# Optimization experiments

Measured on AMD Instinct MI355X. Metric: run time of the kernel, lower is better.

Reference implementation:

```python
import jax, jax.numpy as jnp
import numpy as np

N = 50000      # nodes
E = 1600000    # directed edges (before self-loops)
H = 4          # heads for conv2/conv3


def feast(x, src, dst, W, u, c, b, heads, out_ch):
    """PyG FeaStConv: q = softmax((x_j - x_i) @ u + c) over heads,
    msg = sum_h q_h * (x_j @ W_h), mean-aggregated over in-neighbors, + bias.
    src/dst already include self-loops."""
    xj = x[src]                                   # [E', in]
    xi = x[dst]                                   # [E', in]
    q = jax.nn.softmax((xj - xi) @ u + c, axis=1)            # [E', H]
    t = (xj @ W).reshape(-1, heads, out_ch)                  # [E', H, out]
    m = jnp.einsum('ehc,eh->ec', t, q)                       # [E', out]
    s = jax.ops.segment_sum(m, dst, num_segments=N)          # [N, out]
    deg = jax.ops.segment_sum(jnp.ones((src.shape[0],), x.dtype), dst, num_segments=N)
    return s / jnp.maximum(deg, 1.0)[:, None] + b


def _glorot(k, shape):
    fan_in, fan_out = shape[0], shape[1] if len(shape) > 1 else shape[0]
    lim = np.sqrt(6.0 / (fan_in + fan_out))
    return jax.random.uniform(k, shape, jnp.float32, -lim, lim)


def setup_inputs() -> dict:
    key = jax.random.key(0)
    ks = jax.random.split(key, 32)
    d = {}
    d['x'] = jax.random.normal(ks[0], (N, 16), jnp.float32)
    d['edge_index'] = jax.random.randint(ks[1], (2, E), 0, N, jnp.int32)
    # conv2: 16->16, H=4 ; conv3: 16->16, H=4
    d['W2'] = _glorot(ks[2], (16, H * 16)); d['u2'] = _glorot(ks[3], (16, H))
    d['c2'] = jnp.zeros((H,), jnp.float32); d['b2'] = jnp.zeros((16,), jnp.float32)
    d['W3'] = _glorot(ks[4], (16, H * 16)); d['u3'] = _glorot(ks[5], (16, H))
    d['c3'] = jnp.zeros((H,), jnp.float32); d['b3'] = jnp.zeros((16,), jnp.float32)
    # conv4: 16->16 H=1 ; conv5: 16->32 H=1 ; conv6: 32->64 H=1
    d['W4'] = _glorot(ks[6], (16, 16)); d['u4'] = _glorot(ks[7], (16, 1))
    d['c4'] = jnp.zeros((1,), jnp.float32); d['b4'] = jnp.zeros((16,), jnp.float32)
    d['W5'] = _glorot(ks[8], (16, 32)); d['u5'] = _glorot(ks[9], (16, 1))
    d['c5'] = jnp.zeros((1,), jnp.float32); d['b5'] = jnp.zeros((32,), jnp.float32)
    d['W6'] = _glorot(ks[10], (32, 64)); d['u6'] = _glorot(ks[11], (32, 1))
    d['c6'] = jnp.zeros((1,), jnp.float32); d['b6'] = jnp.zeros((64,), jnp.float32)
    # MLP head: 64->16->4->1
    d['lw1'] = _glorot(ks[12], (64, 16)); d['lb1'] = jnp.zeros((16,), jnp.float32)
    d['lw2'] = _glorot(ks[13], (16, 4));  d['lb2'] = jnp.zeros((4,), jnp.float32)
    d['lw3'] = _glorot(ks[14], (4, 1));   d['lb3'] = jnp.zeros((1,), jnp.float32)
    return d


def reference(x, edge_index, W2, u2, c2, b2, W3, u3, c3, b3, W4, u4, c4, b4,
               W5, u5, c5, b5, W6, u6, c6, b6, lw1, lb1, lw2, lb2, lw3, lb3):
    loop = jnp.arange(N, dtype=edge_index.dtype)
    src = jnp.concatenate([edge_index[0], loop])   # self-loops (PyG default)
    dst = jnp.concatenate([edge_index[1], loop])
    h = jax.nn.relu(x)
    h = jax.nn.relu(feast(h, src, dst, W2, u2, c2, b2, H, 16))
    h = jax.nn.relu(feast(h, src, dst, W3, u3, c3, b3, H, 16))
    h = jax.nn.relu(feast(h, src, dst, W4, u4, c4, b4, 1, 16))
    h = jax.nn.relu(feast(h, src, dst, W5, u5, c5, b5, 1, 32))
    h = jax.nn.relu(feast(h, src, dst, W6, u6, c6, b6, 1, 64))
    h = jax.nn.relu(h @ lw1 + lb1)   # dropout disabled (eval mode)
    h = jax.nn.relu(h @ lw2 + lb2)
    return jax.nn.sigmoid(h @ lw3 + lb3)
```

## Files before the change

kernel.cpp:

```cpp
#include <hip/hip_runtime.h>
#include <math.h>


#define CAP 96
#define NPB 256
#define BCAP 10240

__global__ void part_count(const int* __restrict__ dst, int E,
                           int* __restrict__ counts, int NB) {
    __shared__ int hist[256];
    for (int i = threadIdx.x; i < 256; i += blockDim.x) hist[i] = 0;
    __syncthreads();
    int nth = gridDim.x * blockDim.x;
    int tid = blockIdx.x * blockDim.x + threadIdx.x;
    int E4 = E >> 2;
    const int4* dst4 = (const int4*)dst;
    for (int e4 = tid; e4 < E4; e4 += nth) {
        int4 d = dst4[e4];
        atomicAdd(&hist[d.x >> 8], 1);
        atomicAdd(&hist[d.y >> 8], 1);
        atomicAdd(&hist[d.z >> 8], 1);
        atomicAdd(&hist[d.w >> 8], 1);
    }
    for (int e = (E4 << 2) + tid; e < E; e += nth)
        atomicAdd(&hist[dst[e] >> 8], 1);
    __syncthreads();
    for (int b = threadIdx.x; b < NB; b += blockDim.x)
        counts[b * NPB + blockIdx.x] = hist[b];
}

__global__ void part_scan(int* __restrict__ counts, int* __restrict__ bucketCnt) {
    __shared__ int s[NPB];
    int b = blockIdx.x;
    int t = threadIdx.x;
    int v = counts[b * NPB + t];
    s[t] = v;
    __syncthreads();
    for (int off = 1; off < NPB; off <<= 1) {
        int x = (t >= off) ? s[t - off] : 0;
        __syncthreads();
        s[t] += x;
        __syncthreads();
    }
    counts[b * NPB + t] = s[t] - v;
    if (t == NPB - 1) bucketCnt[b] = s[t];
}

__global__ void part_scatter(const int* __restrict__ src, const int* __restrict__ dst,
                             int E, const int* __restrict__ counts,
                             unsigned int* __restrict__ barr, int NB) {
    __shared__ int cur[256];
    for (int b = threadIdx.x; b < NB; b += blockDim.x)
        cur[b] = counts[b * NPB + blockIdx.x];
    __syncthreads();
    int nth = gridDim.x * blockDim.x;
    int tid = blockIdx.x * blockDim.x + threadIdx.x;
    int E4 = E >> 2;
    const int4* dst4 = (const int4*)dst;
    const int4* src4 = (const int4*)src;
    for (int e4 = tid; e4 < E4; e4 += nth) {
        int4 d = dst4[e4];
        int4 s = src4[e4];
        int p0 = atomicAdd(&cur[d.x >> 8], 1);
        barr[(size_t)(d.x >> 8) * BCAP + p0] = ((unsigned)(d.x & 255) << 16) | (unsigned)s.x;
        int p1 = atomicAdd(&cur[d.y >> 8], 1);
        barr[(size_t)(d.y >> 8) * BCAP + p1] = ((unsigned)(d.y & 255) << 16) | (unsigned)s.y;
        int p2 = atomicAdd(&cur[d.z >> 8], 1);
        barr[(size_t)(d.z >> 8) * BCAP + p2] = ((unsigned)(d.z & 255) << 16) | (unsigned)s.z;
        int p3 = atomicAdd(&cur[d.w >> 8], 1);
        barr[(size_t)(d.w >> 8) * BCAP + p3] = ((unsigned)(d.w & 255) << 16) | (unsigned)s.w;
    }
    for (int e = (E4 << 2) + tid; e < E; e += nth) {
        int d = dst[e];
        int pos = atomicAdd(&cur[d >> 8], 1);
        barr[(size_t)(d >> 8) * BCAP + pos] = ((unsigned)(d & 255) << 16) | (unsigned)src[e];
    }
}

__global__ void build_rows(const unsigned int* __restrict__ barr,
                           const int* __restrict__ bucketCnt,
                           int* __restrict__ padded, int* __restrict__ cnt, int N) {
    __shared__ int c[256];
    int b = blockIdx.x;
    int lo = b << 8;
    int nNodes = min(256, N - lo);
    for (int i = threadIdx.x; i < nNodes; i += blockDim.x) c[i] = 0;
    __syncthreads();
    int tot = bucketCnt[b];
    const unsigned int* be = barr + (size_t)b * BCAP;
    for (int e = threadIdx.x; e < tot; e += blockDim.x) {
        unsigned int pk = be[e];
        int dl = (int)(pk >> 16);
        int s  = (int)(pk & 0xFFFFu);
        int slot = atomicAdd(&c[dl], 1);
        padded[(size_t)(lo + dl) * CAP + slot] = s;
    }
    __syncthreads();
    for (int i = threadIdx.x; i < nNodes; i += blockDim.x) cnt[lo + i] = c[i];
}

template <bool RELU_IN>
__global__ void prep_h4(const float* __restrict__ h, const float* __restrict__ W,
                        const float* __restrict__ u, const float* __restrict__ cvec,
                        float4* __restrict__ Tt, float4* __restrict__ a4,
                        float4* __restrict__ b4, int N) {
    int t = blockIdx.x * blockDim.x + threadIdx.x;
    int i = t >> 4, c = t & 15;
    if (i >= N) return;
    const float4* hp = (const float4*)(h + (size_t)i * 16);
    float4 q0 = hp[0], q1 = hp[1], q2 = hp[2], q3 = hp[3];
    float hv[16] = {q0.x, q0.y, q0.z, q0.w, q1.x, q1.y, q1.z, q1.w,
                    q2.x, q2.y, q2.z, q2.w, q3.x, q3.y, q3.z, q3.w};
    if (RELU_IN) {
        #pragma unroll
        for (int k = 0; k < 16; ++k) hv[k] = fmaxf(hv[k], 0.f);
    }
    float4 tv = {0.f, 0.f, 0.f, 0.f};
    #pragma unroll
    for (int k = 0; k < 16; ++k) {
        const float* Wk = W + k * 64 + c;
        tv.x = fmaf(hv[k], Wk[0],  tv.x);
        tv.y = fmaf(hv[k], Wk[16], tv.y);
        tv.z = fmaf(hv[k], Wk[32], tv.z);
        tv.w = fmaf(hv[k], Wk[48], tv.w);
    }
    Tt[(size_t)i * 16 + c] = tv;
    float p0 = 0.f, p1 = 0.f, p2 = 0.f, p3 = 0.f;
    #pragma unroll
    for (int k = 0; k < 16; ++k) {
        const float* uk = u + k * 4;
        p0 = fmaf(hv[k], uk[0], p0);
        p1 = fmaf(hv[k], uk[1], p1);
        p2 = fmaf(hv[k], uk[2], p2);
        p3 = fmaf(hv[k], uk[3], p3);
    }
    if (c == 0) {
        float z0 = p0 + cvec[0], z1 = p1 + cvec[1];
        float z2 = p2 + cvec[2], z3 = p3 + cvec[3];
        float A = fmaxf(fmaxf(z0, z1), fmaxf(z2, z3));
        float4 av = {__expf(z0 - A), __expf(z1 - A), __expf(z2 - A), __expf(z3 - A)};
        a4[i] = av;
        float B = fminf(fminf(p0, p1), fminf(p2, p3));
        float4 bv = {__expf(B - p0), __expf(B - p1), __expf(B - p2), __expf(B - p3)};
        b4[i] = bv;
    }
}

__global__ void row_h4(const int* __restrict__ cnt, const int* __restrict__ padded,
                       const float4* __restrict__ a4, const float4* __restrict__ b4,
                       const float4* __restrict__ Tt, const float* __restrict__ bvec,
                       float* __restrict__ out, int N) {
    int wid = (blockIdx.x * blockDim.x + threadIdx.x) >> 6;
    int lane = threadIdx.x & 63;
    if (wid >= N) return;
    const int i = wid;
    const int j = lane >> 4, c = lane & 15;
    const int nE = cnt[i];
    const int base = i * CAP;
    const float4 bv = b4[i];
    float acc = 0.f;
    for (int e = j; e < nE; e += 4) {
        int s = padded[base + e];
        float4 av = a4[s];
        float4 tv = Tt[(size_t)s * 16 + c];
        float w0 = av.x * bv.x, w1 = av.y * bv.y;
        float w2 = av.z * bv.z, w3 = av.w * bv.w;
        float sum = (w0 + w1) + (w2 + w3);
        float inv = __builtin_amdgcn_rcpf(sum);
        float dot = fmaf(w0, tv.x, fmaf(w1, tv.y, fmaf(w2, tv.z, w3 * tv.w)));
        acc = fmaf(dot, inv, acc);
    }
    acc += __shfl_xor(acc, 16);
    acc += __shfl_xor(acc, 32);
    if (lane < 16) {
        float4 av = a4[i];
        float4 tv = Tt[(size_t)i * 16 + c];
        float w0 = av.x * bv.x, w1 = av.y * bv.y;
        float w2 = av.z * bv.z, w3 = av.w * bv.w;
        float sum = (w0 + w1) + (w2 + w3);
        float inv = __builtin_amdgcn_rcpf(sum);
        float sval = fmaf(w0, tv.x, fmaf(w1, tv.y, fmaf(w2, tv.z, w3 * tv.w))) * inv;
        out[(size_t)i * 16 + c] = fmaxf((acc + sval) / (float)(nE + 1) + bvec[c], 0.f);
    }
}

template <int IN, int OUT>
__global__ void row_lin(const int* __restrict__ cnt, const int* __restrict__ padded,
                        const float* __restrict__ h, const float* __restrict__ Wm,
                        const float* __restrict__ bvec, float* __restrict__ out, int N) {
    constexpr int QUADS = IN / 4;
    constexpr int GRPS = 64 / QUADS;
    int wid = (blockIdx.x * blockDim.x + threadIdx.x) >> 6;
    int lane = threadIdx.x & 63;
    if (wid >= N) return;
    const int i = wid;
    const int sub = lane & (QUADS - 1);
    const int g = lane / QUADS;
    const int nE = cnt[i];
    const int base = i * CAP;
    const float4* h4 = (const float4*)h;
    float4 acc = {0.f, 0.f, 0.f, 0.f};
    for (int e = g; e < nE; e += GRPS) {
        int s = padded[base + e];
        float4 v = h4[(size_t)s * QUADS + sub];
        acc.x += v.x; acc.y += v.y; acc.z += v.z; acc.w += v.w;
    }
    #pragma unroll
    for (int mask = QUADS; mask < 64; mask <<= 1) {
        acc.x += __shfl_xor(acc.x, mask);
        acc.y += __shfl_xor(acc.y, mask);
        acc.z += __shfl_xor(acc.z, mask);
        acc.w += __shfl_xor(acc.w, mask);
    }
    float invd = 1.0f / (float)(nE + 1);
    float4 sv = h4[(size_t)i * QUADS + sub];
    float4 m;
    m.x = (acc.x + sv.x) * invd;
    m.y = (acc.y + sv.y) * invd;
    m.z = (acc.z + sv.z) * invd;
    m.w = (acc.w + sv.w) * invd;
    int o = (lane < OUT) ? lane : 0;
    float oacc = bvec[o];
    #pragma unroll
    for (int q = 0; q < QUADS; ++q) {
        float m0 = __shfl(m.x, q);
        float m1 = __shfl(m.y, q);
        float m2 = __shfl(m.z, q);
        float m3 = __shfl(m.w, q);
        oacc = fmaf(m0, Wm[(4 * q + 0) * OUT + o], oacc);
        oacc = fmaf(m1, Wm[(4 * q + 1) * OUT + o], oacc);
        oacc = fmaf(m2, Wm[(4 * q + 2) * OUT + o], oacc);
        oacc = fmaf(m3, Wm[(4 * q + 3) * OUT + o], oacc);
    }
    if (lane < OUT) out[(size_t)i * OUT + lane] = fmaxf(oacc, 0.f);
}

__global__ void mlp_kernel(const float* __restrict__ h,
                           const float* __restrict__ lw1, const float* __restrict__ lb1,
                           const float* __restrict__ lw2, const float* __restrict__ lb2,
                           const float* __restrict__ lw3, const float* __restrict__ lb3,
                           float* __restrict__ out, int N) {
    int i = blockIdx.x * blockDim.x + threadIdx.x;
    if (i >= N) return;
    float a1[16];
    #pragma unroll
    for (int o = 0; o < 16; ++o) a1[o] = lb1[o];
    const float4* h4 = (const float4*)(h + (size_t)i * 64);
    #pragma unroll 4
    for (int k4 = 0; k4 < 16; ++k4) {
        float4 v = h4[k4];
        int k = k4 * 4;
        #pragma unroll
        for (int o = 0; o < 16; ++o) {
            a1[o] += v.x * lw1[(k + 0) * 16 + o];
            a1[o] += v.y * lw1[(k + 1) * 16 + o];
            a1[o] += v.z * lw1[(k + 2) * 16 + o];
            a1[o] += v.w * lw1[(k + 3) * 16 + o];
        }
    }
    float a2[4];
    #pragma unroll
    for (int j = 0; j < 4; ++j) a2[j] = lb2[j];
    #pragma unroll
    for (int o = 0; o < 16; ++o) {
        float v = fmaxf(a1[o], 0.f);
        #pragma unroll
        for (int j = 0; j < 4; ++j) a2[j] += v * lw2[o * 4 + j];
    }
    float z = lb3[0];
    #pragma unroll
    for (int j = 0; j < 4; ++j) z += fmaxf(a2[j], 0.f) * lw3[j];
    out[i] = 1.0f / (1.0f + __expf(-z));
}

extern "C" void kernel_launch(void* const* d_in, const int* in_sizes, int n_in,
                              void* d_out, int out_size, void* d_ws, size_t ws_size,
                              hipStream_t stream) {
    const float* x  = (const float*)d_in[0];
    const int*   ei = (const int*)d_in[1];
    const int E = in_sizes[1] / 2;
    const int N = in_sizes[0] / 16;
    const int* src = ei;
    const int* dst = ei + E;

    const float* W2 = (const float*)d_in[2];
    const float* u2 = (const float*)d_in[3];
    const float* c2 = (const float*)d_in[4];
    const float* b2 = (const float*)d_in[5];
    const float* W3 = (const float*)d_in[6];
    const float* u3 = (const float*)d_in[7];
    const float* c3 = (const float*)d_in[8];
    const float* b3 = (const float*)d_in[9];
    const float* W4 = (const float*)d_in[10];
    const float* b4v = (const float*)d_in[13];
    const float* W5 = (const float*)d_in[14];
    const float* b5 = (const float*)d_in[17];
    const float* W6 = (const float*)d_in[18];
    const float* b6 = (const float*)d_in[21];
    const float* lw1 = (const float*)d_in[22];
    const float* lb1 = (const float*)d_in[23];
    const float* lw2 = (const float*)d_in[24];
    const float* lb2 = (const float*)d_in[25];
    const float* lw3 = (const float*)d_in[26];
    const float* lb3 = (const float*)d_in[27];

    const int NB = (N + 255) >> 8;

    float* bufA = (float*)d_ws;
    float* bufB = bufA + (size_t)N * 64;
    float4* Tt  = (float4*)(bufB + (size_t)N * 64);
    float4* a4  = Tt + (size_t)N * 16;
    float4* b4  = a4 + N;
    int*   padded    = (int*)(b4 + N);
    int*   cnt       = padded + (size_t)N * CAP;
    unsigned int* barr = (unsigned int*)(cnt + N);
    int*   counts    = (int*)(barr + (size_t)NB * BCAP);
    int*   bucketCnt = counts + NB * NPB;

    const int BS = 256;
    const int rowBlocks = (N + 3) / 4;
    const int prepBlocks = (N * 16 + BS - 1) / BS;

    part_count<<<NPB, BS, 0, stream>>>(dst, E, counts, NB);
    part_scan<<<NB, NPB, 0, stream>>>(counts, bucketCnt);
    part_scatter<<<NPB, BS, 0, stream>>>(src, dst, E, counts, barr, NB);
    build_rows<<<NB, BS, 0, stream>>>(barr, bucketCnt, padded, cnt, N);

    prep_h4<true><<<prepBlocks, BS, 0, stream>>>(x, W2, u2, c2, Tt, a4, b4, N);
    row_h4<<<rowBlocks, BS, 0, stream>>>(cnt, padded, a4, b4, Tt, b2, bufB, N);

    prep_h4<false><<<prepBlocks, BS, 0, stream>>>(bufB, W3, u3, c3, Tt, a4, b4, N);
    row_h4<<<rowBlocks, BS, 0, stream>>>(cnt, padded, a4, b4, Tt, b3, bufA, N);

    row_lin<16, 16><<<rowBlocks, BS, 0, stream>>>(cnt, padded, bufA, W4, b4v, bufB, N);

    row_lin<16, 32><<<rowBlocks, BS, 0, stream>>>(cnt, padded, bufB, W5, b5, bufA, N);

    row_lin<32, 64><<<rowBlocks, BS, 0, stream>>>(cnt, padded, bufA, W6, b6, bufB, N);

    mlp_kernel<<<(N + BS - 1) / BS, BS, 0, stream>>>(bufB, lw1, lb1, lw2, lb2, lw3, lb3,
                                                     (float*)d_out, N);
}
```

Measured before the change: 284.1 us.

## Store gathered neighbor features and transformed features in fp16 to halve gather traffic

The per-node transformed features Tt used by the multi-head layers are now stored as half precision, and each layer also writes an fp16 copy of its output that the next mean-aggregation layer gathers from. The row_lin gather is restructured so each lane owns 8 halves (16 bytes) instead of a float4, which reduces per-edge random-read bytes. Self-loop terms still use fp32. This trades precision for less memory traffic on the dominant irregular gathers, at the cost of extra fp16 output writes and possible accuracy loss.

New measurement: 311.7 us. +9.7%, slower.

```diff
diff --git a/kernel.cpp b/kernel.cpp
--- a/kernel.cpp
+++ b/kernel.cpp
@@ -1,10 +1,14 @@
 #include <hip/hip_runtime.h>
+#include <hip/hip_fp16.h>
 #include <math.h>
 
 
 #define CAP 96
 #define NPB 256
 #define BCAP 10240
+
+struct alignas(8)  H4 { __half2 lo, hi; };
+struct alignas(16) H8 { __half2 a, b, c, d; };
 
 __global__ void part_count(const int* __restrict__ dst, int E,
                            int* __restrict__ counts, int NB) {
@@ -102,7 +106,7 @@
 template <bool RELU_IN>
 __global__ void prep_h4(const float* __restrict__ h, const float* __restrict__ W,
                         const float* __restrict__ u, const float* __restrict__ cvec,
-                        float4* __restrict__ Tt, float4* __restrict__ a4,
+                        H4* __restrict__ TtH, float4* __restrict__ a4,
                         float4* __restrict__ b4, int N) {
     int t = blockIdx.x * blockDim.x + threadIdx.x;
     int i = t >> 4, c = t & 15;
@@ -124,7 +128,10 @@
         tv.z = fmaf(hv[k], Wk[32], tv.z);
         tv.w = fmaf(hv[k], Wk[48], tv.w);
     }
-    Tt[(size_t)i * 16 + c] = tv;
+    H4 o;
+    o.lo = __floats2half2_rn(tv.x, tv.y);
+    o.hi = __floats2half2_rn(tv.z, tv.w);
+    TtH[(size_t)i * 16 + c] = o;
     float p0 = 0.f, p1 = 0.f, p2 = 0.f, p3 = 0.f;
     #pragma unroll
     for (int k = 0; k < 16; ++k) {
@@ -148,8 +155,8 @@
 
 __global__ void row_h4(const int* __restrict__ cnt, const int* __restrict__ padded,
                        const float4* __restrict__ a4, const float4* __restrict__ b4,
-                       const float4* __restrict__ Tt, const float* __restrict__ bvec,
-                       float* __restrict__ out, int N) {
+                       const H4* __restrict__ TtH, const float* __restrict__ bvec,
+                       float* __restrict__ out, __half* __restrict__ out16, int N) {
     int wid = (blockIdx.x * blockDim.x + threadIdx.x) >> 6;
     int lane = threadIdx.x & 63;
     if (wid >= N) return;
@@ -162,77 +169,92 @@
     for (int e = j; e < nE; e += 4) {
         int s = padded[base + e];
         float4 av = a4[s];
-        float4 tv = Tt[(size_t)s * 16 + c];
+        H4 tvh = TtH[(size_t)s * 16 + c];
+        float2 tl = __half22float2(tvh.lo);
+        float2 th = __half22float2(tvh.hi);
         float w0 = av.x * bv.x, w1 = av.y * bv.y;
         float w2 = av.z * bv.z, w3 = av.w * bv.w;
         float sum = (w0 + w1) + (w2 + w3);
         float inv = __builtin_amdgcn_rcpf(sum);
-        float dot = fmaf(w0, tv.x, fmaf(w1, tv.y, fmaf(w2, tv.z, w3 * tv.w)));
+        float dot = fmaf(w0, tl.x, fmaf(w1, tl.y, fmaf(w2, th.x, w3 * th.y)));
         acc = fmaf(dot, inv, acc);
     }
     acc += __shfl_xor(acc, 16);
     acc += __shfl_xor(acc, 32);
     if (lane < 16) {
         float4 av = a4[i];
-        float4 tv = Tt[(size_t)i * 16 + c];
+        H4 tvh = TtH[(size_t)i * 16 + c];
+        float2 tl = __half22float2(tvh.lo);
+        float2 th = __half22float2(tvh.hi);
         float w0 = av.x * bv.x, w1 = av.y * bv.y;
         float w2 = av.z * bv.z, w3 = av.w * bv.w;
         float sum = (w0 + w1) + (w2 + w3);
         float inv = __builtin_amdgcn_rcpf(sum);
-        float sval = fmaf(w0, tv.x, fmaf(w1, tv.y, fmaf(w2, tv.z, w3 * tv.w))) * inv;
-        out[(size_t)i * 16 + c] = fmaxf((acc + sval) / (float)(nE + 1) + bvec[c], 0.f);
+        float sval = fmaf(w0, tl.x, fmaf(w1, tl.y, fmaf(w2, th.x, w3 * th.y))) * inv;
+        float r = fmaxf((acc + sval) / (float)(nE + 1) + bvec[c], 0.f);
+        out[(size_t)i * 16 + c] = r;
+        if (out16) out16[(size_t)i * 16 + c] = __float2half(r);
     }
 }
 
 template <int IN, int OUT>
 __global__ void row_lin(const int* __restrict__ cnt, const int* __restrict__ padded,
-                        const float* __restrict__ h, const float* __restrict__ Wm,
-                        const float* __restrict__ bvec, float* __restrict__ out, int N) {
-    constexpr int QUADS = IN / 4;
-    constexpr int GRPS = 64 / QUADS;
+                        const float* __restrict__ h32, const __half* __restrict__ h16,
+                        const float* __restrict__ Wm, const float* __restrict__ bvec,
+                        float* __restrict__ out, __half* __restrict__ out16, int N) {
+    constexpr int OWN = IN / 8;
+    constexpr int SH = (OWN == 2) ? 1 : 2;
+    constexpr int GRPS = 64 / OWN;
     int wid = (blockIdx.x * blockDim.x + threadIdx.x) >> 6;
     int lane = threadIdx.x & 63;
     if (wid >= N) return;
     const int i = wid;
-    const int sub = lane & (QUADS - 1);
-    const int g = lane / QUADS;
+    const int sub = lane & (OWN - 1);
+    const int g = lane >> SH;
     const int nE = cnt[i];
     const int base = i * CAP;
-    const float4* h4 = (const float4*)h;
-    float4 acc = {0.f, 0.f, 0.f, 0.f};
+    const H8* hp = (const H8*)h16;
+    float acc[8] = {0.f, 0.f, 0.f, 0.f, 0.f, 0.f, 0.f, 0.f};
     for (int e = g; e < nE; e += GRPS) {
         int s = padded[base + e];
-        float4 v = h4[(size_t)s * QUADS + sub];
-        acc.x += v.x; acc.y += v.y; acc.z += v.z; acc.w += v.w;
-    }
-    #pragma unroll
-    for (int mask = QUADS; mask < 64; mask <<= 1) {
-        acc.x += __shfl_xor(acc.x, mask);
-        acc.y += __shfl_xor(acc.y, mask);
-        acc.z += __shfl_xor(acc.z, mask);
-        acc.w += __shfl_xor(acc.w, mask);
+        H8 v = hp[(size_t)s * OWN + sub];
+        float2 f0 = __half22float2(v.a);
+        float2 f1 = __half22float2(v.b);
+        float2 f2 = __half22float2(v.c);
+        float2 f3 = __half22float2(v.d);
+        acc[0] += f0.x; acc[1] += f0.y;
+        acc[2] += f1.x; acc[3] += f1.y;
+        acc[4] += f2.x; acc[5] += f2.y;
+        acc[6] += f3.x; acc[7] += f3.y;
+    }
+    if (g == 0) {
+        const float4* s4 = (const float4*)(h32 + (size_t)i * IN);
+        float4 v0 = s4[sub * 2], v1 = s4[sub * 2 + 1];
+        acc[0] += v0.x; acc[1] += v0.y; acc[2] += v0.z; acc[3] += v0.w;
+        acc[4] += v1.x; acc[5] += v1.y; acc[6] += v1.z; acc[7] += v1.w;
+    }
+    #pragma unroll
+    for (int mask = OWN; mask < 64; mask <<= 1) {
+        #pragma unroll
+        for (int k = 0; k < 8; ++k) acc[k] += __shfl_xor(acc[k], mask);
     }
     float invd = 1.0f / (float)(nE + 1);
-    float4 sv = h4[(size_t)i * QUADS + sub];
-    float4 m;
-    m.x = (acc.x + sv.x) * invd;
-    m.y = (acc.y + sv.y) * invd;
-    m.z = (acc.z + sv.z) * invd;
-    m.w = (acc.w + sv.w) * invd;
+    float m[8];
+    #pragma unroll
+    for (int k = 0; k < 8; ++k) m[k] = acc[k] * invd;
     int o = (lane < OUT) ? lane : 0;
     float oacc = bvec[o];
     #pragma unroll
-    for (int q = 0; q < QUADS; ++q) {
-        float m0 = __shfl(m.x, q);
-        float m1 = __shfl(m.y, q);
-        float m2 = __shfl(m.z, q);
-        float m3 = __shfl(m.w, q);
-        oacc = fmaf(m0, Wm[(4 * q + 0) * OUT + o], oacc);
-        oacc = fmaf(m1, Wm[(4 * q + 1) * OUT + o], oacc);
-        oacc = fmaf(m2, Wm[(4 * q + 2) * OUT + o], oacc);
-        oacc = fmaf(m3, Wm[(4 * q + 3) * OUT + o], oacc);
-    }
-    if (lane < OUT) out[(size_t)i * OUT + lane] = fmaxf(oacc, 0.f);
+    for (int q = 0; q < OWN; ++q) {
+        #pragma unroll
+        for (int k = 0; k < 8; ++k)
+            oacc = fmaf(__shfl(m[k], q), Wm[(8 * q + k) * OUT + o], oacc);
+    }
+    if (lane < OUT) {
+        float r = fmaxf(oacc, 0.f);
+        out[(size_t)i * OUT + lane] = r;
+        if (out16) out16[(size_t)i * OUT + lane] = __float2half(r);
+    }
 }
 
 __global__ void mlp_kernel(const float* __restrict__ h,
@@ -308,10 +330,12 @@
 
     float* bufA = (float*)d_ws;
     float* bufB = bufA + (size_t)N * 64;
-    float4* Tt  = (float4*)(bufB + (size_t)N * 64);
-    float4* a4  = Tt + (size_t)N * 16;
+    float4* a4  = (float4*)(bufB + (size_t)N * 64);
     float4* b4  = a4 + N;
-    int*   padded    = (int*)(b4 + N);
+    H4*    TtH  = (H4*)(b4 + N);
+    __half* bufAh = (__half*)(TtH + (size_t)N * 16);
+    __half* bufBh = bufAh + (size_t)N * 32;
+    int*   padded    = (int*)(bufBh + (size_t)N * 16);
     int*   cnt       = padded + (size_t)N * CAP;
     unsigned int* barr = (unsigned int*)(cnt + N);
     int*   counts    = (int*)(barr + (size_t)NB * BCAP);
@@ -326,17 +350,20 @@
     part_scatter<<<NPB, BS, 0, stream>>>(src, dst, E, counts, barr, NB);
     build_rows<<<NB, BS, 0, stream>>>(barr, bucketCnt, padded, cnt, N);
 
-    prep_h4<true><<<prepBlocks, BS, 0, stream>>>(x, W2, u2, c2, Tt, a4, b4, N);
-    row_h4<<<rowBlocks, BS, 0, stream>>>(cnt, padded, a4, b4, Tt, b2, bufB, N);
-
-    prep_h4<false><<<prepBlocks, BS, 0, stream>>>(bufB, W3, u3, c3, Tt, a4, b4, N);
-    row_h4<<<rowBlocks, BS, 0, stream>>>(cnt, padded, a4, b4, Tt, b3, bufA, N);
-
-    row_lin<16, 16><<<rowBlocks, BS, 0, stream>>>(cnt, padded, bufA, W4, b4v, bufB, N);
-
-    row_lin<16, 32><<<rowBlocks, BS, 0, stream>>>(cnt, padded, bufB, W5, b5, bufA, N);
-
-    row_lin<32, 64><<<rowBlocks, BS, 0, stream>>>(cnt, padded, bufA, W6, b6, bufB, N);
+    prep_h4<true><<<prepBlocks, BS, 0, stream>>>(x, W2, u2, c2, TtH, a4, b4, N);
+    row_h4<<<rowBlocks, BS, 0, stream>>>(cnt, padded, a4, b4, TtH, b2, bufB, nullptr, N);
+
+    prep_h4<false><<<prepBlocks, BS, 0, stream>>>(bufB, W3, u3, c3, TtH, a4, b4, N);
+    row_h4<<<rowBlocks, BS, 0, stream>>>(cnt, padded, a4, b4, TtH, b3, bufA, bufAh, N);
+
+    row_lin<16, 16><<<rowBlocks, BS, 0, stream>>>(cnt, padded, bufA, bufAh, W4, b4v,
+                                                  bufB, bufBh, N);
+
+    row_lin<16, 32><<<rowBlocks, BS, 0, stream>>>(cnt, padded, bufB, bufBh, W5, b5,
+                                                  bufA, bufAh, N);
+
+    row_lin<32, 64><<<rowBlocks, BS, 0, stream>>>(cnt, padded, bufA, bufAh, W6, b6,
+                                                  bufB, nullptr, N);
 
     mlp_kernel<<<(N + BS - 1) / BS, BS, 0, stream>>>(bufB, lw1, lb1, lw2, lb2, lw3, lb3,
                                                      (float*)d_out, N);
```
